# Kernel optimization log

Measured on AMD Instinct MI355X. Metric: run time of the kernel, lower is better.

Reference implementation:

```python
import jax, jax.numpy as jnp
import numpy as np

HEADS = 16

def setup_inputs() -> dict:
    key = jax.random.key(0)
    ks = jax.random.split(key, 7)
    B, S, E = 2, 2048, 1024
    return {
        "query": jax.random.normal(ks[0], (B, S, E), dtype=jnp.float32),
        "key": jax.random.normal(ks[1], (B, S, E), dtype=jnp.float32),
        "value": jax.random.normal(ks[2], (B, S, E), dtype=jnp.float32),
        "Wqkv": jax.random.normal(ks[3], (E, 3 * E), dtype=jnp.float32) * (E ** -0.5),
        "bqkv": jax.random.normal(ks[4], (3 * E,), dtype=jnp.float32) * 0.02,
        "Wproj": jax.random.normal(ks[5], (E, E), dtype=jnp.float32) * (E ** -0.5),
        "bproj": jax.random.normal(ks[6], (E,), dtype=jnp.float32) * 0.02,
    }

def reference(query, key, value, Wqkv, bqkv, Wproj, bproj):
    # key/value args are unused in the original forward (overwritten by QKV split)
    B, S, E = query.shape
    H = HEADS
    hd = E // H
    qkv = query @ Wqkv + bqkv                     # [B, S, 3E]
    qkv = qkv.reshape(B, S, H, 3 * hd).transpose(0, 2, 1, 3)  # [B, H, S, 3hd]
    q = qkv[..., :hd]
    k = qkv[..., hd:2 * hd]
    v = qkv[..., 2 * hd:]
    qk = jnp.einsum("bhqd,bhkd->bhqk", q, k)
    # faithful quirk: original divides by head_dim**-0.5, i.e. multiplies by sqrt(hd)
    scaled = qk / (hd ** -0.5)
    attn = jax.nn.softmax(scaled, axis=-1)        # dropout p=0 -> identity
    out = jnp.einsum("bhqk,bhkd->bhqd", attn, v)  # [B, H, S, hd]
    out = out.transpose(0, 2, 1, 3).reshape(B, S, E)
    return out @ Wproj + bproj
```

## Files before the change

kernel.cpp:

```cpp
#include <hip/hip_runtime.h>
#include <hip/hip_bf16.h>
#include <stdint.h>

typedef __attribute__((ext_vector_type(8))) _Float16 f16x8;
typedef __attribute__((ext_vector_type(4))) _Float16 f16x4;
typedef __attribute__((ext_vector_type(4))) float f32x4;

static constexpr int BATCH = 2;
static constexpr int SEQ = 2048;
static constexpr int EMB = 1024;
static constexpr int NH = 16;
static constexpr int HD_ = 64;

#define AS1 __attribute__((address_space(1)))
#define AS3 __attribute__((address_space(3)))

__device__ __forceinline__ void gload_lds16(const void* g, void* l) {
  __builtin_amdgcn_global_load_lds((const AS1 uint32_t*)g, (AS3 uint32_t*)l, 16, 0, 0);
}

__device__ __forceinline__ f32x4 mfma16(f16x8 a, f16x8 b, f32x4 c) {
  return __builtin_amdgcn_mfma_f32_16x16x32_f16(a, b, c, 0, 0, 0);
}

__device__ __forceinline__ f16x8 swzread(const _Float16* base, int row, int blk) {
  return *(const f16x8*)((const char*)base + row * 128 +
                         ((blk * 16) ^ ((row & 7) << 4)));
}

__global__ __launch_bounds__(256) void k_convert_split(const float* __restrict__ in,
                                                       _Float16* __restrict__ oh,
                                                       _Float16* __restrict__ ol,
                                                       int n4) {
  int idx = blockIdx.x * 256 + threadIdx.x;
  if (idx >= n4) return;
  float4 v = reinterpret_cast<const float4*>(in)[idx];
  const float* f = reinterpret_cast<const float*>(&v);
  _Float16 h[4], l[4];
#pragma unroll
  for (int i = 0; i < 4; ++i) {
    h[i] = (_Float16)f[i];
    l[i] = (_Float16)(f[i] - (float)h[i]);
  }
  reinterpret_cast<uint2*>(oh)[idx] = *reinterpret_cast<uint2*>(h);
  reinterpret_cast<uint2*>(ol)[idx] = *reinterpret_cast<uint2*>(l);
}

template <int PERM>
__global__ __launch_bounds__(256) void k_transpose(const float* __restrict__ in,
                                                   _Float16* __restrict__ out, int R,
                                                   int C) {
  __shared__ float tile[32][33];
  const int t = threadIdx.x;
  const int tr = t >> 5, tc = t & 31;
  const int r0 = blockIdx.y * 32, c0 = blockIdx.x * 32;
#pragma unroll
  for (int rr = 0; rr < 32; rr += 8)
    tile[tr + rr][tc] = in[(size_t)(r0 + tr + rr) * C + c0 + tc];
  __syncthreads();
#pragma unroll
  for (int rr = 0; rr < 32; rr += 8) {
    const int c = c0 + tr + rr;
    int d = c;
    if constexpr (PERM) {
      const int h = c / 192, r = c - h * 192;
      d = (r < 64) ? h * 64 + r
                   : (r < 128 ? 1024 + h * 64 + (r - 64) : 2048 + h * 64 + (r - 128));
    }
    out[(size_t)d * R + r0 + tc] = (_Float16)tile[tc][tr + rr];
  }
}

__global__ __launch_bounds__(256) void k_gemm_qkv(
    const _Float16* __restrict__ Ah, const _Float16* __restrict__ Al,
    const _Float16* __restrict__ Bt, const float* __restrict__ bias,
    _Float16* __restrict__ oq, _Float16* __restrict__ ok,
    _Float16* __restrict__ ov) {
  constexpr int K = EMB;
  __shared__ _Float16 AsH[2][128 * 32];
  __shared__ _Float16 AsL[2][128 * 32];
  __shared__ _Float16 Bs[2][128 * 32];
  const int t = threadIdx.x;
  const int l = t & 63, w = t >> 6;
  const int lr = l & 15, lg = l >> 4;
  const int wr = w >> 1, wc = w & 1;
  const int m0 = blockIdx.y * 128, n0 = blockIdx.x * 128;
  const bool splitb = (n0 < 2048);

  auto stage = [&](int buf, int k0) {
#pragma unroll
    for (int j = 0; j < 2; ++j) {
      const int c = t + 256 * j;
      const int row = c >> 2, cb = c & 3;
      const size_t ga = (size_t)(m0 + row) * K + k0 + cb * 8;
      const size_t gb = (size_t)(n0 + row) * K + k0 + cb * 8;
      gload_lds16(Ah + ga, &AsH[buf][c * 8]);
      gload_lds16(Bt + gb, &Bs[buf][c * 8]);
      if (splitb) gload_lds16(Al + ga, &AsL[buf][c * 8]);
    }
  };

  f32x4 acc[4][4];
#pragma unroll
  for (int m = 0; m < 4; ++m)
#pragma unroll
    for (int n = 0; n < 4; ++n) acc[m][n] = f32x4{0.f, 0.f, 0.f, 0.f};

  stage(0, 0);
  const int NT = K / 32;
  int cur = 0;
  for (int kt = 0; kt < NT; ++kt) {
    __syncthreads();
    if (kt + 1 < NT) stage(cur ^ 1, (kt + 1) * 32);
    f16x8 afh[4], afl[4], bf[4];
#pragma unroll
    for (int m = 0; m < 4; ++m) {
      const int off = (wr * 64 + m * 16 + lr) * 32 + lg * 8;
      afh[m] = *(const f16x8*)&AsH[cur][off];
      if (splitb) afl[m] = *(const f16x8*)&AsL[cur][off];
    }
#pragma unroll
    for (int n = 0; n < 4; ++n)
      bf[n] = *(const f16x8*)&Bs[cur][(wc * 64 + n * 16 + lr) * 32 + lg * 8];
#pragma unroll
    for (int m = 0; m < 4; ++m)
#pragma unroll
      for (int n = 0; n < 4; ++n) {
        acc[m][n] = mfma16(afh[m], bf[n], acc[m][n]);
        if (splitb) acc[m][n] = mfma16(afl[m], bf[n], acc[m][n]);
      }
    cur ^= 1;
  }

#pragma unroll
  for (int m = 0; m < 4; ++m) {
#pragma unroll
    for (int n = 0; n < 4; ++n) {
#pragma unroll
      for (int i = 0; i < 4; ++i) {
        const int row = m0 + wr * 64 + m * 16 + lg * 4 + i;
        const int col = n0 + wc * 64 + n * 16 + lr;
        const int cc = col & 1023;
        const int h = cc >> 6, r = cc & 63;
        const int sec = col >> 10;
        const float v = acc[m][n][i] + bias[h * 192 + sec * 64 + r];
        const int b = row >> 11, s = row & (SEQ - 1);
        if (sec == 0)
          oq[(((size_t)b * NH + h) * SEQ + s) * HD_ + r] =
              (_Float16)(v * 11.5415603f);
        else if (sec == 1)
          ok[(((size_t)b * NH + h) * SEQ + s) * HD_ + r] = (_Float16)v;
        else
          ov[(((size_t)b * NH + h) * HD_ + r) * SEQ + s] = (_Float16)v;
      }
    }
  }
}

__global__ __launch_bounds__(256) void k_gemm_proj(const _Float16* __restrict__ A,
                                                   const _Float16* __restrict__ Bt,
                                                   const float* __restrict__ bias,
                                                   float* __restrict__ of) {
  constexpr int K = EMB, N = EMB;
  __shared__ _Float16 As[2][128 * 32];
  __shared__ _Float16 Bs[2][128 * 32];
  const int t = threadIdx.x;
  const int l = t & 63, w = t >> 6;
  const int lr = l & 15, lg = l >> 4;
  const int wr = w >> 1, wc = w & 1;
  const int m0 = blockIdx.y * 128, n0 = blockIdx.x * 128;

  auto stage = [&](int buf, int k0) {
#pragma unroll
    for (int j = 0; j < 2; ++j) {
      const int c = t + 256 * j;
      const int row = c >> 2, cb = c & 3;
      gload_lds16(A + (size_t)(m0 + row) * K + k0 + cb * 8, &As[buf][c * 8]);
      gload_lds16(Bt + (size_t)(n0 + row) * K + k0 + cb * 8, &Bs[buf][c * 8]);
    }
  };

  f32x4 acc[4][4];
#pragma unroll
  for (int m = 0; m < 4; ++m)
#pragma unroll
    for (int n = 0; n < 4; ++n) acc[m][n] = f32x4{0.f, 0.f, 0.f, 0.f};

  stage(0, 0);
  const int NT = K / 32;
  int cur = 0;
  for (int kt = 0; kt < NT; ++kt) {
    __syncthreads();
    if (kt + 1 < NT) stage(cur ^ 1, (kt + 1) * 32);
    f16x8 af[4], bf[4];
#pragma unroll
    for (int m = 0; m < 4; ++m)
      af[m] = *(const f16x8*)&As[cur][(wr * 64 + m * 16 + lr) * 32 + lg * 8];
#pragma unroll
    for (int n = 0; n < 4; ++n)
      bf[n] = *(const f16x8*)&Bs[cur][(wc * 64 + n * 16 + lr) * 32 + lg * 8];
#pragma unroll
    for (int m = 0; m < 4; ++m)
#pragma unroll
      for (int n = 0; n < 4; ++n) acc[m][n] = mfma16(af[m], bf[n], acc[m][n]);
    cur ^= 1;
  }

#pragma unroll
  for (int m = 0; m < 4; ++m)
#pragma unroll
    for (int n = 0; n < 4; ++n)
#pragma unroll
      for (int i = 0; i < 4; ++i) {
        const int row = m0 + wr * 64 + m * 16 + lg * 4 + i;
        const int col = n0 + wc * 64 + n * 16 + lr;
        of[(size_t)row * N + col] = acc[m][n][i] + bias[col];
      }
}

__global__ __launch_bounds__(512) void k_attn(const _Float16* __restrict__ qs,
                                              const _Float16* __restrict__ ks,
                                              const _Float16* __restrict__ vt,
                                              _Float16* __restrict__ ao) {
  __shared__ _Float16 Kt[2][64][64];
  __shared__ _Float16 Vt[2][64][64];
  __shared__ _Float16 Pl[8][16][64];
  const int t = threadIdx.x;
  const int l = t & 63, w = t >> 6;
  const int lr = l & 15, lg = l >> 4;
  const int id = blockIdx.x;
  const int xc = id & 7, m_ = id >> 3;
  const int bh = xc + 8 * (m_ >> 4);
  const int qb = (m_ & 15) * 128 + w * 16;

  const size_t qoff = ((size_t)bh * SEQ + qb + lr) * HD_;
  const f16x8 qf0 = *(const f16x8*)(qs + qoff + lg * 8);
  const f16x8 qf1 = *(const f16x8*)(qs + qoff + 32 + lg * 8);

  const _Float16* kbase = ks + (size_t)bh * SEQ * HD_;
  const _Float16* vbase = vt + (size_t)bh * HD_ * SEQ;

  const int srow = t >> 3, scb = t & 7;
  auto stage = [&](const int buf, const int kv0) {
    gload_lds16(kbase + (size_t)(kv0 + srow) * HD_ + (scb ^ (srow & 7)) * 8,
                &Kt[buf][srow][scb * 8]);
    gload_lds16(vbase + (size_t)srow * SEQ + kv0 + (scb ^ (srow & 7)) * 8,
                &Vt[buf][srow][scb * 8]);
  };

  stage(0, 0);

  float mr = -1e30f, lsum = 0.f;
  f32x4 oacc[4];
#pragma unroll
  for (int n = 0; n < 4; ++n) oacc[n] = f32x4{0.f, 0.f, 0.f, 0.f};

  const int NT = SEQ / 64;
  for (int it = 0; it < NT; ++it) {
    const int cur = it & 1;
    __syncthreads();
    if (it + 1 < NT) stage(cur ^ 1, (it + 1) * 64);

    f32x4 sa[4];
    __builtin_amdgcn_s_setprio(1);
#pragma unroll
    for (int t4 = 0; t4 < 4; ++t4) {
      const int r = t4 * 16 + lr;
      const f16x8 kf0 = swzread(&Kt[cur][0][0], r, lg);
      const f16x8 kf1 = swzread(&Kt[cur][0][0], r, lg + 4);
      f32x4 s = mfma16(kf0, qf0, f32x4{0.f, 0.f, 0.f, 0.f});
      sa[t4] = mfma16(kf1, qf1, s);
    }
    __builtin_amdgcn_s_setprio(0);

    float t01 = fmaxf(fmaxf(sa[0][0], sa[0][1]), fmaxf(sa[0][2], sa[0][3]));
    float t23 = fmaxf(fmaxf(sa[1][0], sa[1][1]), fmaxf(sa[1][2], sa[1][3]));
    float t45 = fmaxf(fmaxf(sa[2][0], sa[2][1]), fmaxf(sa[2][2], sa[2][3]));
    float t67 = fmaxf(fmaxf(sa[3][0], sa[3][1]), fmaxf(sa[3][2], sa[3][3]));
    float tm = fmaxf(fmaxf(t01, t23), fmaxf(t45, t67));
    tm = fmaxf(tm, __shfl_xor(tm, 16));
    tm = fmaxf(tm, __shfl_xor(tm, 32));

    if (__any(tm > mr + 8.0f)) {
      const float nm = fmaxf(mr, tm);
      const float corr = exp2f(mr - nm);
      mr = nm;
      lsum *= corr;
      float cb4[4];
#pragma unroll
      for (int i = 0; i < 4; ++i)
        cb4[i] = __shfl(corr, (l & 48) + ((l >> 4) << 2) + i);
#pragma unroll
      for (int n = 0; n < 4; ++n)
#pragma unroll
        for (int i = 0; i < 4; ++i) oacc[n][i] *= cb4[i];
    }

    float ts = 0.f;
    char* plbase = (char*)&Pl[w][0][0];
#pragma unroll
    for (int t4 = 0; t4 < 4; ++t4) {
      f16x4 pp;
#pragma unroll
      for (int i = 0; i < 4; ++i) {
        const float p = exp2f(sa[t4][i] - mr);
        ts += p;
        pp[i] = (_Float16)p;
      }
      *(f16x4*)(plbase + lr * 128 + ((t4 * 32 + lg * 8) ^ ((lr & 7) << 4))) = pp;
    }
    ts += __shfl_xor(ts, 16);
    ts += __shfl_xor(ts, 32);
    lsum += ts;

    const f16x8 aP0 = swzread(&Pl[w][0][0], lr, lg);
    const f16x8 aP1 = swzread(&Pl[w][0][0], lr, lg + 4);
    __builtin_amdgcn_s_setprio(1);
#pragma unroll
    for (int n = 0; n < 4; ++n) {
      const int d = n * 16 + lr;
      const f16x8 bv0 = swzread(&Vt[cur][0][0], d, lg);
      const f16x8 bv1 = swzread(&Vt[cur][0][0], d, lg + 4);
      oacc[n] = mfma16(aP0, bv0, oacc[n]);
      oacc[n] = mfma16(aP1, bv1, oacc[n]);
    }
    __builtin_amdgcn_s_setprio(0);
  }

  float ls4[4];
#pragma unroll
  for (int i = 0; i < 4; ++i)
    ls4[i] = __shfl(lsum, (l & 48) + ((l >> 4) << 2) + i);
  const int b = bh >> 4, h = bh & 15;
#pragma unroll
  for (int n = 0; n < 4; ++n)
#pragma unroll
    for (int i = 0; i < 4; ++i) {
      const int row = qb + ((l >> 4) << 2) + i;
      ao[((size_t)b * SEQ + row) * EMB + h * HD_ + n * 16 + lr] =
          (_Float16)(oacc[n][i] / ls4[i]);
    }
}

extern "C" void kernel_launch(void* const* d_in, const int* in_sizes, int n_in,
                              void* d_out, int out_size, void* d_ws, size_t ws_size,
                              hipStream_t stream) {
  const float* query = (const float*)d_in[0];
  const float* Wqkv = (const float*)d_in[3];
  const float* bqkv = (const float*)d_in[4];
  const float* Wproj = (const float*)d_in[5];
  const float* bproj = (const float*)d_in[6];
  float* out = (float*)d_out;

  char* ws = (char*)d_ws;
  const size_t MB = 1024 * 1024;
  _Float16* q_hi    = (_Float16*)(ws + 0);
  _Float16* q_lo    = (_Float16*)(ws + 8 * MB);
  _Float16* Wqkv_t  = (_Float16*)(ws + 16 * MB);
  _Float16* q_s     = (_Float16*)(ws + 24 * MB);
  _Float16* k_s     = (_Float16*)(ws + 32 * MB);
  _Float16* v_t     = (_Float16*)(ws + 40 * MB);
  _Float16* a_o     = (_Float16*)(ws + 0);
  _Float16* Wproj_t = (_Float16*)(ws + 8 * MB);

  const int M = BATCH * SEQ;
  k_convert_split<<<(M * EMB / 4 + 255) / 256, 256, 0, stream>>>(query, q_hi, q_lo,
                                                                 M * EMB / 4);
  k_transpose<1><<<dim3(3 * EMB / 32, EMB / 32), 256, 0, stream>>>(Wqkv, Wqkv_t, EMB,
                                                                   3 * EMB);
  k_gemm_qkv<<<dim3(24, M / 128), 256, 0, stream>>>(q_hi, q_lo, Wqkv_t, bqkv, q_s, k_s,
                                                    v_t);
  k_transpose<0><<<dim3(EMB / 32, EMB / 32), 256, 0, stream>>>(Wproj, Wproj_t, EMB, EMB);
  k_attn<<<dim3(512), 512, 0, stream>>>(q_s, k_s, v_t, a_o);
  k_gemm_proj<<<dim3(EMB / 128, M / 128), 256, 0, stream>>>(a_o, Wproj_t, bproj, out);
}
```

Before: 167.9 us.

## Split attention KV range across two blocks and add combine kernel

```diff
diff --git a/kernel.cpp b/kernel.cpp
--- a/kernel.cpp
+++ b/kernel.cpp
@@ -132,26 +132,32 @@
     cur ^= 1;
   }
 
+  const int sec = n0 >> 10;
 #pragma unroll
   for (int m = 0; m < 4; ++m) {
 #pragma unroll
     for (int n = 0; n < 4; ++n) {
-#pragma unroll
-      for (int i = 0; i < 4; ++i) {
-        const int row = m0 + wr * 64 + m * 16 + lg * 4 + i;
-        const int col = n0 + wc * 64 + n * 16 + lr;
-        const int cc = col & 1023;
-        const int h = cc >> 6, r = cc & 63;
-        const int sec = col >> 10;
-        const float v = acc[m][n][i] + bias[h * 192 + sec * 64 + r];
-        const int b = row >> 11, s = row & (SEQ - 1);
-        if (sec == 0)
-          oq[(((size_t)b * NH + h) * SEQ + s) * HD_ + r] =
-              (_Float16)(v * 11.5415603f);
-        else if (sec == 1)
-          ok[(((size_t)b * NH + h) * SEQ + s) * HD_ + r] = (_Float16)v;
-        else
-          ov[(((size_t)b * NH + h) * HD_ + r) * SEQ + s] = (_Float16)v;
+      const int col = n0 + wc * 64 + n * 16 + lr;
+      const int cc = col & 1023;
+      const int h = cc >> 6, r = cc & 63;
+      const float bv = bias[h * 192 + sec * 64 + r];
+      const int row0 = m0 + wr * 64 + m * 16 + lg * 4;
+      const int b = row0 >> 11, s0 = row0 & (SEQ - 1);
+      if (sec == 2) {
+        f16x4 vv;
+#pragma unroll
+        for (int i = 0; i < 4; ++i) vv[i] = (_Float16)(acc[m][n][i] + bv);
+        *(f16x4*)&ov[(((size_t)b * NH + h) * HD_ + r) * SEQ + s0] = vv;
+      } else {
+#pragma unroll
+        for (int i = 0; i < 4; ++i) {
+          const float v = acc[m][n][i] + bv;
+          const size_t dst = (((size_t)b * NH + h) * SEQ + s0 + i) * HD_ + r;
+          if (sec == 0)
+            oq[dst] = (_Float16)(v * 11.5415603f);
+          else
+            ok[dst] = (_Float16)v;
+        }
       }
     }
   }
@@ -218,10 +224,10 @@
       }
 }
 
-__global__ __launch_bounds__(512) void k_attn(const _Float16* __restrict__ qs,
-                                              const _Float16* __restrict__ ks,
-                                              const _Float16* __restrict__ vt,
-                                              _Float16* __restrict__ ao) {
+__global__ __launch_bounds__(512) void k_attn(
+    const _Float16* __restrict__ qs, const _Float16* __restrict__ ks,
+    const _Float16* __restrict__ vt, _Float16* __restrict__ op,
+    float* __restrict__ marr, float* __restrict__ larr) {
   __shared__ _Float16 Kt[2][64][64];
   __shared__ _Float16 Vt[2][64][64];
   __shared__ _Float16 Pl[8][16][64];
@@ -230,8 +236,10 @@
   const int lr = l & 15, lg = l >> 4;
   const int id = blockIdx.x;
   const int xc = id & 7, m_ = id >> 3;
-  const int bh = xc + 8 * (m_ >> 4);
-  const int qb = (m_ & 15) * 128 + w * 16;
+  const int kvh = m_ & 1;
+  const int bh = xc + 8 * (m_ >> 5);
+  const int qb = ((m_ >> 1) & 15) * 128 + w * 16;
+  const int kvbase = kvh * (SEQ / 2);
 
   const size_t qoff = ((size_t)bh * SEQ + qb + lr) * HD_;
   const f16x8 qf0 = *(const f16x8*)(qs + qoff + lg * 8);
@@ -248,18 +256,18 @@
                 &Vt[buf][srow][scb * 8]);
   };
 
-  stage(0, 0);
+  stage(0, kvbase);
 
   float mr = -1e30f, lsum = 0.f;
   f32x4 oacc[4];
 #pragma unroll
   for (int n = 0; n < 4; ++n) oacc[n] = f32x4{0.f, 0.f, 0.f, 0.f};
 
-  const int NT = SEQ / 64;
+  const int NT = SEQ / 128;
   for (int it = 0; it < NT; ++it) {
     const int cur = it & 1;
     __syncthreads();
-    if (it + 1 < NT) stage(cur ^ 1, (it + 1) * 64);
+    if (it + 1 < NT) stage(cur ^ 1, kvbase + (it + 1) * 64);
 
     f32x4 sa[4];
     __builtin_amdgcn_s_setprio(1);
@@ -327,19 +335,46 @@
     __builtin_amdgcn_s_setprio(0);
   }
 
-  float ls4[4];
-#pragma unroll
-  for (int i = 0; i < 4; ++i)
-    ls4[i] = __shfl(lsum, (l & 48) + ((l >> 4) << 2) + i);
+  const size_t mlbase = ((size_t)kvh * 32 + bh) * SEQ + qb;
+  if (l < 16) {
+    marr[mlbase + l] = mr;
+    larr[mlbase + l] = lsum;
+  }
+  _Float16* opb = op + (size_t)kvh * BATCH * SEQ * EMB;
   const int b = bh >> 4, h = bh & 15;
 #pragma unroll
   for (int n = 0; n < 4; ++n)
 #pragma unroll
     for (int i = 0; i < 4; ++i) {
       const int row = qb + ((l >> 4) << 2) + i;
-      ao[((size_t)b * SEQ + row) * EMB + h * HD_ + n * 16 + lr] =
-          (_Float16)(oacc[n][i] / ls4[i]);
-    }
+      opb[((size_t)b * SEQ + row) * EMB + h * HD_ + n * 16 + lr] =
+          (_Float16)oacc[n][i];
+    }
+}
+
+__global__ __launch_bounds__(256) void k_combine(const _Float16* __restrict__ op,
+                                                 const float* __restrict__ marr,
+                                                 const float* __restrict__ larr,
+                                                 _Float16* __restrict__ ao) {
+  const int idx = blockIdx.x * 256 + threadIdx.x;
+  const int e8 = idx & 127;
+  const size_t rs = (size_t)(idx >> 7);
+  const int h = e8 >> 3;
+  const int b = (int)(rs >> 11);
+  const size_t s = rs & (SEQ - 1);
+  const size_t mi = ((size_t)b * NH + h) * SEQ + s;
+  const float m1 = marr[mi], l1 = larr[mi];
+  const float m2 = marr[(size_t)32 * SEQ + mi], l2 = larr[(size_t)32 * SEQ + mi];
+  const float mx = fmaxf(m1, m2);
+  const float w1 = exp2f(m1 - mx), w2 = exp2f(m2 - mx);
+  const float inv = 1.0f / (l1 * w1 + l2 * w2);
+  const f16x8 o1 = ((const f16x8*)op)[idx];
+  const f16x8 o2 = ((const f16x8*)op)[idx + (BATCH * SEQ * EMB / 8)];
+  f16x8 r;
+#pragma unroll
+  for (int j = 0; j < 8; ++j)
+    r[j] = (_Float16)(((float)o1[j] * w1 + (float)o2[j] * w2) * inv);
+  ((f16x8*)ao)[idx] = r;
 }
 
 extern "C" void kernel_launch(void* const* d_in, const int* in_sizes, int n_in,
@@ -360,8 +395,11 @@
   _Float16* q_s     = (_Float16*)(ws + 24 * MB);
   _Float16* k_s     = (_Float16*)(ws + 32 * MB);
   _Float16* v_t     = (_Float16*)(ws + 40 * MB);
-  _Float16* a_o     = (_Float16*)(ws + 0);
-  _Float16* Wproj_t = (_Float16*)(ws + 8 * MB);
+  _Float16* op      = (_Float16*)(ws + 0);
+  _Float16* Wproj_t = (_Float16*)(ws + 48 * MB);
+  float*    marr    = (float*)(ws + 50 * MB);
+  float*    larr    = (float*)(ws + 50 * MB + 512 * 1024);
+  _Float16* a_o     = (_Float16*)(ws + 51 * MB);
 
   const int M = BATCH * SEQ;
   k_convert_split<<<(M * EMB / 4 + 255) / 256, 256, 0, stream>>>(query, q_hi, q_lo,
@@ -371,6 +409,7 @@
   k_gemm_qkv<<<dim3(24, M / 128), 256, 0, stream>>>(q_hi, q_lo, Wqkv_t, bqkv, q_s, k_s,
                                                     v_t);
   k_transpose<0><<<dim3(EMB / 32, EMB / 32), 256, 0, stream>>>(Wproj, Wproj_t, EMB, EMB);
-  k_attn<<<dim3(512), 512, 0, stream>>>(q_s, k_s, v_t, a_o);
+  k_attn<<<dim3(1024), 512, 0, stream>>>(q_s, k_s, v_t, op, marr, larr);
+  k_combine<<<dim3(BATCH * SEQ * EMB / 8 / 256), 256, 0, stream>>>(op, marr, larr, a_o);
   k_gemm_proj<<<dim3(EMB / 128, M / 128), 256, 0, stream>>>(a_o, Wproj_t, bproj, out);
 }
```

Measured after the change: 165.6 us. About the same (-1.4%).
